# Kernel optimization log

Measured on AMD Instinct MI355X. Metric: run time of the kernel, lower is better.

The kernel has to match this reference:

```python
import jax, jax.numpy as jnp
import numpy as np

N = 100000   # nodes
E = 1600000  # edges
G = 512      # graphs
IN_F = 128
HID = 64
EPS = 1e-5


def setup_inputs() -> dict:
    key = jax.random.key(0)
    ks = jax.random.split(key, 16)
    x = jax.random.normal(ks[0], (N, IN_F), dtype=jnp.float32)
    edge_index = jax.random.randint(ks[1], (2, E), 0, N, dtype=jnp.int64)
    batch = jnp.sort(jax.random.randint(ks[2], (N,), 0, G, dtype=jnp.int64))
    s = 0.05
    return {
        'x': x, 'edge_index': edge_index, 'batch': batch,
        'W1': jax.random.normal(ks[3], (IN_F, HID), jnp.float32) * s,
        'b1': jax.random.normal(ks[4], (HID,), jnp.float32) * s,
        'g1': jax.random.uniform(ks[5], (HID,), jnp.float32),
        'be1': jax.random.normal(ks[6], (HID,), jnp.float32) * s,
        'rm1': jnp.zeros((HID,), jnp.float32),
        'rv1': jnp.ones((HID,), jnp.float32),
        'W2': jax.random.normal(ks[7], (HID, HID), jnp.float32) * s,
        'b2': jax.random.normal(ks[8], (HID,), jnp.float32) * s,
        'g2': jax.random.uniform(ks[9], (HID,), jnp.float32),
        'be2': jax.random.normal(ks[10], (HID,), jnp.float32) * s,
        'rm2': jnp.zeros((HID,), jnp.float32),
        'rv2': jnp.ones((HID,), jnp.float32),
        'Wh1': jax.random.normal(ks[11], (2 * HID, HID), jnp.float32) * s,
        'bh1': jax.random.normal(ks[12], (HID,), jnp.float32) * s,
        'Wh2': jax.random.normal(ks[13], (HID, HID // 2), jnp.float32) * s,
        'bh2': jnp.zeros((HID // 2,), jnp.float32),
        'Wh3': jax.random.normal(ks[14], (HID // 2, 1), jnp.float32) * s,
        'bh3': jnp.zeros((1,), jnp.float32),
    }


def _gcn(h, W, b, src, dst):
    # GCNConv with added self-loops and symmetric D^{-1/2} A D^{-1/2} normalization
    hw = h @ W                                   # [N, HID]
    deg = jnp.ones((N,), hw.dtype).at[dst].add(1.0)  # in-degree + self-loop
    dinv = jax.lax.rsqrt(deg)
    norm = dinv[src] * dinv[dst]                 # [E]
    agg = jax.ops.segment_sum(hw[src] * norm[:, None], dst, num_segments=N)
    return agg + hw * (dinv * dinv)[:, None] + b  # self-loop term + bias


def _bn(x, g, b, rm, rv):
    return (x - rm) * jax.lax.rsqrt(rv + EPS) * g + b


def reference(x, edge_index, batch, W1, b1, g1, be1, rm1, rv1,
              W2, b2, g2, be2, rm2, rv2, Wh1, bh1, Wh2, bh2, Wh3, bh3):
    src, dst = edge_index[0], edge_index[1]
    # layer 0 (no residual: dim change 128 -> 64)
    h = jax.nn.relu(_bn(_gcn(x, W1, b1, src, dst), g1, be1, rm1, rv1))
    # layer 1 with residual
    h = h + jax.nn.relu(_bn(_gcn(h, W2, b2, src, dst), g2, be2, rm2, rv2))
    # global mean + max pooling per graph
    ones = jnp.ones((N,), h.dtype)
    cnt = jnp.maximum(jax.ops.segment_sum(ones, batch, num_segments=G), 1.0)
    h_mean = jax.ops.segment_sum(h, batch, num_segments=G) / cnt[:, None]
    h_max = jax.ops.segment_max(h, batch, num_segments=G)
    hg = jnp.concatenate([h_mean, h_max], axis=-1)   # [G, 2*HID]
    # MLP head (dropout disabled in eval)
    z = jax.nn.relu(hg @ Wh1 + bh1)
    z = jax.nn.relu(z @ Wh2 + bh2)
    out = z @ Wh3 + bh3
    return jax.nn.sigmoid(out).squeeze(-1)           # [G]
```

## Files before the change

kernel.cpp:

```cpp
#include <hip/hip_runtime.h>
#include <math.h>

#define NN 100000
#define EE 1600000
#define GG 512
#define INF_ 128
#define HID 64
#define EPS 1e-5f

#define NBUK 391
#define P1_TILES 98
#define SETUP_B 25
#define POOL_WORDS (GG * 64 * 2 + GG)
#define ZERO_B ((POOL_WORDS + 255) / 256)

typedef unsigned int uint32;
typedef __attribute__((ext_vector_type(8))) short bf16x8;
typedef __attribute__((ext_vector_type(4))) float f32x4;

static __device__ inline uint32 f2bf(float f) {
    uint32 u = __float_as_uint(f);
    return (u + 0x7FFFu + ((u >> 16) & 1u)) >> 16;
}
static __device__ inline float bf_lo(uint32 u) { return __uint_as_float(u << 16); }
static __device__ inline float bf_hi(uint32 u) { return __uint_as_float(u & 0xFFFF0000u); }



__global__ __launch_bounds__(256) void k_hist1(const int* __restrict__ ei,
        int* __restrict__ hblk,
        const float* b1, const float* g1, const float* be1,
        const float* rm1, const float* rv1,
        const float* b2, const float* g2, const float* be2,
        const float* rm2, const float* rv2, float* sc,
        const float* W1, uint32* Wt1b, const float* W2, uint32* Wt2b,
        uint32* hwb, float* poolz) {
    int b = blockIdx.x, t = threadIdx.x;
    if (b < P1_TILES) {
        __shared__ int h[NBUK];
        for (int i = t; i < NBUK; i += 256) h[i] = 0;
        __syncthreads();
        const int4* dst4 = (const int4*)(ei + EE);
        int base4 = b * 4096;
        for (int j = 0; j < 16; ++j) {
            int i4 = base4 + j * 256 + t;
            if (i4 < EE / 4) {
                int4 d = dst4[i4];
                atomicAdd(&h[d.x >> 8], 1);
                atomicAdd(&h[d.y >> 8], 1);
                atomicAdd(&h[d.z >> 8], 1);
                atomicAdd(&h[d.w >> 8], 1);
            }
        }
        __syncthreads();
        for (int i = t; i < NBUK; i += 256) hblk[i * P1_TILES + b] = h[i];
    } else if (b < P1_TILES + SETUP_B) {
        int i = (b - P1_TILES) * 256 + t;
        if (i < 4096) {
            int n = i >> 6, kp = (i & 63) * 2;
            Wt1b[i] = f2bf(W1[(size_t)kp * 64 + n]) |
                      (f2bf(W1[(size_t)(kp + 1) * 64 + n]) << 16);
        } else if (i < 6144) {
            int j = i - 4096;
            int n = j >> 5, kp = (j & 31) * 2;
            Wt2b[j] = f2bf(W2[(size_t)kp * 64 + n]) |
                      (f2bf(W2[(size_t)(kp + 1) * 64 + n]) << 16);
        } else if (i < 6208) {
            int l = i - 6144;
            float s1 = g1[l] * rsqrtf(rv1[l] + EPS);
            sc[l]       = s1;
            sc[64 + l]  = (b1[l] - rm1[l]) * s1 + be1[l];
            float s2 = g2[l] * rsqrtf(rv2[l] + EPS);
            sc[128 + l] = s2;
            sc[192 + l] = (b2[l] - rm2[l]) * s2 + be2[l];
        } else if (i < 6240) {
            hwb[(size_t)NN * 32 + (i - 6208)] = 0u;
        }
    } else {
        int i = (b - P1_TILES - SETUP_B) * 256 + t;
        if (i < POOL_WORDS) poolz[i] = 0.f;
    }
}

__global__ void k_scan2(const int* __restrict__ hblk, int* __restrict__ bbase,
                        int* __restrict__ rbase, int* __restrict__ offs) {
    __shared__ int wsum[8];
    int t = threadIdx.x;
    int lane = t & 63, w = t >> 6;
    int c = 0;
    if (t < NBUK)
        for (int b = 0; b < P1_TILES; ++b) c += hblk[t * P1_TILES + b];
    int v = c;
    for (int d = 1; d < 64; d <<= 1) { int n = __shfl_up(v, d); if (lane >= d) v += n; }
    if (lane == 63) wsum[w] = v;
    __syncthreads();
    int pre = 0;
    for (int q = 0; q < w; ++q) pre += wsum[q];
    int excl = pre + v - c;
    if (t <= NBUK) bbase[t] = excl;
    if (t == 0) offs[NN] = EE;
    if (t < NBUK) {
        int run = excl;
        for (int b = 0; b < P1_TILES; ++b) {
            rbase[t * P1_TILES + b] = run;
            run += hblk[t * P1_TILES + b];
        }
    }
}

__global__ __launch_bounds__(256) void k_p1b(const int* __restrict__ ei,
                                             const int* __restrict__ rbase,
                                             uint32* __restrict__ pairs) {
    __shared__ int h[NBUK];
    int b = blockIdx.x, t = threadIdx.x;
    for (int i = t; i < NBUK; i += 256) h[i] = rbase[i * P1_TILES + b];
    __syncthreads();
    const int4* src4 = (const int4*)ei;
    const int4* dst4 = (const int4*)(ei + EE);
    int base4 = b * 4096;
    for (int j = 0; j < 16; ++j) {
        int i4 = base4 + j * 256 + t;
        if (i4 < EE / 4) {
            int4 d = dst4[i4];
            int4 s = src4[i4];
            int p0 = atomicAdd(&h[d.x >> 8], 1);
            pairs[p0] = ((uint32)s.x << 8) | (uint32)(d.x & 255);
            int p1 = atomicAdd(&h[d.y >> 8], 1);
            pairs[p1] = ((uint32)s.y << 8) | (uint32)(d.y & 255);
            int p2 = atomicAdd(&h[d.z >> 8], 1);
            pairs[p2] = ((uint32)s.z << 8) | (uint32)(d.z & 255);
            int p3 = atomicAdd(&h[d.w >> 8], 1);
            pairs[p3] = ((uint32)s.w << 8) | (uint32)(d.w & 255);
        }
    }
}

__global__ __launch_bounds__(256) void k_p2(const uint32* __restrict__ pairs,
                                            const int* __restrict__ bbase,
                                            int* __restrict__ offs, float* __restrict__ dinv,
                                            int* __restrict__ col) {
    int b = blockIdx.x, t = threadIdx.x;
    int nbase = b << 8;
    int ebase = bbase[b], eend = bbase[b + 1];
    int m = eend - ebase;
    __shared__ int cnt[256];
    __shared__ int wsum[4];
    cnt[t] = 0;
    __syncthreads();
    for (int i = t; i < m; i += 256)
        atomicAdd(&cnt[pairs[ebase + i] & 255u], 1);
    __syncthreads();
    int c = cnt[t];
    int lane = t & 63, w = t >> 6;
    int v = c;
    for (int d = 1; d < 64; d <<= 1) { int n = __shfl_up(v, d); if (lane >= d) v += n; }
    if (lane == 63) wsum[w] = v;
    __syncthreads();
    int pre = 0;
    for (int q = 0; q < w; ++q) pre += wsum[q];
    int excl = pre + v - c;
    int node = nbase + t;
    if (node < NN) {
        offs[node] = ebase + excl;
        dinv[node] = rsqrtf(1.f + (float)c);
    }
    __syncthreads();
    cnt[t] = excl;
    __syncthreads();
    for (int i = t; i < m; i += 256) {
        uint32 u = pairs[ebase + i];
        int loc = atomicAdd(&cnt[u & 255u], 1);
        col[ebase + loc] = (int)(u >> 8);
    }
}

template <int K>
__global__ __launch_bounds__(256) void k_gemm_mfma(const float* __restrict__ X,
                                                   const uint32* __restrict__ Wtb,
                                                   const float* __restrict__ dinv,
                                                   uint32* __restrict__ outb, int nrows) {
    constexpr int KP = K + 8;
    __shared__ alignas(16) unsigned short Al[64 * KP];
    __shared__ alignas(16) unsigned short Bl[64 * KP];
    int tid = threadIdx.x;
    for (int i = tid; i < 64 * (K / 2); i += 256) {
        int n = i / (K / 2), kp = i % (K / 2);
        *(uint32*)&Bl[n * KP + kp * 2] = Wtb[i];
    }
    int r0 = blockIdx.x * 64;
    const float* Xb = X + (size_t)r0 * K;
    int limit = (nrows - r0) * K;
    for (int f = tid * 4; f < 64 * K; f += 1024) {
        float4 v = {0.f, 0.f, 0.f, 0.f};
        if (f + 3 < limit) v = *(const float4*)&Xb[f];
        int row = f / K, kpos = f % K;
        ushort4 pk;
        pk.x = (unsigned short)f2bf(v.x);
        pk.y = (unsigned short)f2bf(v.y);
        pk.z = (unsigned short)f2bf(v.z);
        pk.w = (unsigned short)f2bf(v.w);
        *(ushort4*)&Al[row * KP + kpos] = pk;
    }
    __syncthreads();
    int lane = tid & 63, wv = tid >> 6;
    int m = lane & 15, quad = lane >> 4;
    f32x4 acc0 = {0.f, 0.f, 0.f, 0.f}, acc1 = acc0, acc2 = acc0, acc3 = acc0;
    int arow = wv * 16 + m;
#pragma unroll
    for (int k0 = 0; k0 < K; k0 += 32) {
        int koff = k0 + quad * 8;
        bf16x8 a = *(const bf16x8*)&Al[arow * KP + koff];
        bf16x8 b0 = *(const bf16x8*)&Bl[(0 * 16 + m) * KP + koff];
        bf16x8 b1 = *(const bf16x8*)&Bl[(1 * 16 + m) * KP + koff];
        bf16x8 b2 = *(const bf16x8*)&Bl[(2 * 16 + m) * KP + koff];
        bf16x8 b3 = *(const bf16x8*)&Bl[(3 * 16 + m) * KP + koff];
        acc0 = __builtin_amdgcn_mfma_f32_16x16x32_bf16(a, b0, acc0, 0, 0, 0);
        acc1 = __builtin_amdgcn_mfma_f32_16x16x32_bf16(a, b1, acc1, 0, 0, 0);
        acc2 = __builtin_amdgcn_mfma_f32_16x16x32_bf16(a, b2, acc2, 0, 0, 0);
        acc3 = __builtin_amdgcn_mfma_f32_16x16x32_bf16(a, b3, acc3, 0, 0, 0);
    }
    float dsc[4];
#pragma unroll
    for (int reg = 0; reg < 4; ++reg) {
        int row = r0 + wv * 16 + quad * 4 + reg;
        dsc[reg] = (row < nrows) ? dinv[row] : 0.f;
    }
    const float* accs[4] = {(const float*)&acc0, (const float*)&acc1,
                            (const float*)&acc2, (const float*)&acc3};
#pragma unroll
    for (int nt = 0; nt < 4; ++nt) {
#pragma unroll
        for (int reg = 0; reg < 4; ++reg) {
            float val = accs[nt][reg] * dsc[reg];
            float nxt = __shfl_down(val, 1);
            int row = r0 + wv * 16 + quad * 4 + reg;
            if (((m & 1) == 0) && row < nrows)
                outb[(size_t)row * 32 + nt * 8 + (m >> 1)] =
                    f2bf(val) | (f2bf(nxt) << 16);
        }
    }
}

__global__ void k_gcn_gather(const uint32* __restrict__ hwb, const int* __restrict__ col,
                             const int* __restrict__ offs,
                             const float* __restrict__ dinv, const float* __restrict__ scale,
                             const float* __restrict__ shift, const float* __restrict__ resid,
                             float* __restrict__ out) {
    int node = blockIdx.x * 4 + (threadIdx.x >> 6);
    if (node >= NN) return;
    int lane = threadIdx.x & 63;
    int q = lane >> 4;
    int fl = lane & 15;
    const uint2* hw2 = (const uint2*)hwb;
    int e0 = offs[node], e1 = offs[node + 1];
    float di = dinv[node];
    float a0 = 0.f, a1 = 0.f, a2 = 0.f, a3 = 0.f;
    float c0 = 0.f, c1 = 0.f, c2 = 0.f, c3 = 0.f;
    for (int base = e0; base < e1; base += 64) {
        int m = e1 - base; if (m > 64) m = 64;
        int srcv = NN;
        if (lane < m) srcv = col[base + lane];
        for (int j = 0; j < m; j += 16) {
            int sa = __shfl(srcv, j + q);
            int sb = __shfl(srcv, j + 4 + q);
            int sc = __shfl(srcv, j + 8 + q);
            int sd = __shfl(srcv, j + 12 + q);
            uint2 ua = hw2[(size_t)sa * 16 + fl];
            uint2 ub = hw2[(size_t)sb * 16 + fl];
            uint2 uc = hw2[(size_t)sc * 16 + fl];
            uint2 ud = hw2[(size_t)sd * 16 + fl];
            a0 += bf_lo(ua.x); a1 += bf_hi(ua.x); a2 += bf_lo(ua.y); a3 += bf_hi(ua.y);
            c0 += bf_lo(ub.x); c1 += bf_hi(ub.x); c2 += bf_lo(ub.y); c3 += bf_hi(ub.y);
            a0 += bf_lo(uc.x); a1 += bf_hi(uc.x); a2 += bf_lo(uc.y); a3 += bf_hi(uc.y);
            c0 += bf_lo(ud.x); c1 += bf_hi(ud.x); c2 += bf_lo(ud.y); c3 += bf_hi(ud.y);
        }
    }
    a0 += c0; a1 += c1; a2 += c2; a3 += c3;
    a0 += __shfl_xor(a0, 16); a1 += __shfl_xor(a1, 16);
    a2 += __shfl_xor(a2, 16); a3 += __shfl_xor(a3, 16);
    a0 += __shfl_xor(a0, 32); a1 += __shfl_xor(a1, 32);
    a2 += __shfl_xor(a2, 32); a3 += __shfl_xor(a3, 32);
    if (q == 0) {
        uint2 us = hw2[(size_t)node * 16 + fl];
        a0 += bf_lo(us.x); a1 += bf_hi(us.x);
        a2 += bf_lo(us.y); a3 += bf_hi(us.y);
        float4 sc4 = *(const float4*)&scale[4 * fl];
        float4 sh4 = *(const float4*)&shift[4 * fl];
        float v0 = fmaxf(fmaf(a0 * di, sc4.x, sh4.x), 0.f);
        float v1 = fmaxf(fmaf(a1 * di, sc4.y, sh4.y), 0.f);
        float v2 = fmaxf(fmaf(a2 * di, sc4.z, sh4.z), 0.f);
        float v3 = fmaxf(fmaf(a3 * di, sc4.w, sh4.w), 0.f);
        size_t oidx = (size_t)node * 64 + 4 * fl;
        if (resid) {
            float4 rv = *(const float4*)&resid[oidx];
            v0 += rv.x; v1 += rv.y; v2 += rv.z; v3 += rv.w;
        }
        float4 o; o.x = v0; o.y = v1; o.z = v2; o.w = v3;
        *(float4*)&out[oidx] = o;
    }
}

__global__ __launch_bounds__(256) void k_pool(const float* __restrict__ h,
                       const int* __restrict__ batch,
                       float* __restrict__ msum, float* __restrict__ mmax,
                       float* __restrict__ gcnt) {
    int lane = threadIdx.x & 63;
    int wv = threadIdx.x >> 6;
    int i0 = blockIdx.x * 128 + wv * 32;
    if (i0 >= NN) return;
    int i1 = i0 + 32; if (i1 > NN) i1 = NN;
    int cur = batch[i0];
    float sum = 0.f, mx = 0.f; int c = 0;
    for (int i = i0; i < i1; ++i) {
        int g = batch[i];
        if (g != cur) {
            atomicAdd(&msum[cur * 64 + lane], sum);
            atomicMax((unsigned int*)&mmax[cur * 64 + lane], __float_as_uint(mx));
            if (lane == 0) atomicAdd(&gcnt[cur], (float)c);
            sum = 0.f; mx = 0.f; c = 0; cur = g;
        }
        float v = h[(long)i * 64 + lane];
        sum += v; mx = fmaxf(mx, v); ++c;
    }
    atomicAdd(&msum[cur * 64 + lane], sum);
    atomicMax((unsigned int*)&mmax[cur * 64 + lane], __float_as_uint(mx));
    if (lane == 0) atomicAdd(&gcnt[cur], (float)c);
}

__global__ void k_head(const float* __restrict__ msum, const float* __restrict__ mmax,
                       const float* __restrict__ gcnt,
                       const float* __restrict__ Wh1, const float* __restrict__ bh1,
                       const float* __restrict__ Wh2, const float* __restrict__ bh2,
                       const float* __restrict__ Wh3, const float* __restrict__ bh3,
                       float* __restrict__ out) {
    int g = blockIdx.x, t = threadIdx.x;
    __shared__ float hg[128];
    __shared__ float z1[64];
    __shared__ float z2[32];
    float c = fmaxf(gcnt[g], 1.f);
    hg[t]      = msum[g * 64 + t] / c;
    hg[64 + t] = mmax[g * 64 + t];
    __syncthreads();
    float acc = bh1[t];
#pragma unroll 8
    for (int k = 0; k < 128; ++k) acc = fmaf(hg[k], Wh1[k * 64 + t], acc);
    z1[t] = fmaxf(acc, 0.f);
    __syncthreads();
    if (t < 32) {
        float a2 = bh2[t];
#pragma unroll 8
        for (int k = 0; k < 64; ++k) a2 = fmaf(z1[k], Wh2[k * 32 + t], a2);
        z2[t] = fmaxf(a2, 0.f);
    }
    __syncthreads();
    if (t == 0) {
        float a3 = bh3[0];
        for (int k = 0; k < 32; ++k) a3 = fmaf(z2[k], Wh3[k], a3);
        out[g] = 1.f / (1.f + expf(-a3));
    }
}


static inline size_t alignup(size_t x) { return (x + 255) & ~(size_t)255; }

extern "C" void kernel_launch(void* const* d_in, const int* in_sizes, int n_in,
                              void* d_out, int out_size, void* d_ws, size_t ws_size,
                              hipStream_t stream) {
    const float* x   = (const float*)d_in[0];
    const int*   ei  = (const int*)d_in[1];
    const int*   bat = (const int*)d_in[2];
    const float* W1  = (const float*)d_in[3];
    const float* b1  = (const float*)d_in[4];
    const float* g1  = (const float*)d_in[5];
    const float* be1 = (const float*)d_in[6];
    const float* rm1 = (const float*)d_in[7];
    const float* rv1 = (const float*)d_in[8];
    const float* W2  = (const float*)d_in[9];
    const float* b2  = (const float*)d_in[10];
    const float* g2  = (const float*)d_in[11];
    const float* be2 = (const float*)d_in[12];
    const float* rm2 = (const float*)d_in[13];
    const float* rv2 = (const float*)d_in[14];
    const float* Wh1 = (const float*)d_in[15];
    const float* bh1 = (const float*)d_in[16];
    const float* Wh2 = (const float*)d_in[17];
    const float* bh2 = (const float*)d_in[18];
    const float* Wh3 = (const float*)d_in[19];
    const float* bh3 = (const float*)d_in[20];
    float* out = (float*)d_out;

    char* ws = (char*)d_ws;
    size_t o = 0;
    int*   hblk   = (int*)(ws + o);  o = alignup(o + (size_t)P1_TILES * NBUK * 4);
    int*   rbase  = (int*)(ws + o);  o = alignup(o + (size_t)P1_TILES * NBUK * 4);
    int*   bbase  = (int*)(ws + o);  o = alignup(o + (NBUK + 1) * 4);
    int*   offs   = (int*)(ws + o);  o = alignup(o + (NN + 1) * 4);
    uint32* pairs = (uint32*)(ws + o); o = alignup(o + (size_t)EE * 4);
    int*   col    = (int*)(ws + o);  o = alignup(o + (size_t)EE * 4);
    float* dinv   = (float*)(ws + o); o = alignup(o + (size_t)NN * 4);
    float* scb    = (float*)(ws + o); o = alignup(o + 4 * 64 * 4);
    uint32* Wt1b  = (uint32*)(ws + o); o = alignup(o + 64 * (INF_ / 2) * 4);
    uint32* Wt2b  = (uint32*)(ws + o); o = alignup(o + 64 * (HID / 2) * 4);
    float* msum   = (float*)(ws + o); o += (size_t)GG * 64 * 4;
    float* mmax   = (float*)(ws + o); o += (size_t)GG * 64 * 4;
    float* gcnt   = (float*)(ws + o); o += (size_t)GG * 4;
    o = alignup(o);
    uint32* hwb   = (uint32*)(ws + o); o = alignup(o + ((size_t)NN + 1) * 32 * 4);
    float* h      = (float*)(ws + o); o = alignup(o + (size_t)NN * 64 * 4);
    (void)ws_size; (void)n_in; (void)in_sizes; (void)out_size;

    k_hist1<<<P1_TILES + SETUP_B + ZERO_B, 256, 0, stream>>>(
        ei, hblk, b1, g1, be1, rm1, rv1, b2, g2, be2, rm2, rv2, scb,
        W1, Wt1b, W2, Wt2b, hwb, msum);
    k_scan2<<<1, 512, 0, stream>>>(hblk, bbase, rbase, offs);
    k_p1b<<<P1_TILES, 256, 0, stream>>>(ei, rbase, pairs);
    k_p2<<<NBUK, 256, 0, stream>>>(pairs, bbase, offs, dinv, col);

    k_gemm_mfma<INF_><<<(NN + 63) / 64, 256, 0, stream>>>(x, Wt1b, dinv, hwb, NN);
    k_gcn_gather<<<(NN + 3) / 4, 256, 0, stream>>>(hwb, col, offs, dinv,
                                                   scb, scb + 64, nullptr, h);
    k_gemm_mfma<HID><<<(NN + 63) / 64, 256, 0, stream>>>(h, Wt2b, dinv, hwb, NN);
    k_gcn_gather<<<(NN + 3) / 4, 256, 0, stream>>>(hwb, col, offs, dinv,
                                                   scb + 128, scb + 192, h, h);
    k_pool<<<(NN + 127) / 128, 256, 0, stream>>>(h, bat, msum, mmax, gcnt);
    k_head<<<GG, 64, 0, stream>>>(msum, mmax, gcnt, Wh1, bh1, Wh2, bh2, Wh3, bh3, out);
}
```

Measured before the change: 312.2 us.

## Store intermediate node features in bf16 and regather with 32-lane half-wave layout

The hidden activations h are now stored as packed bf16 pairs instead of fp32. The second GEMM reads them directly without conversion, and pooling reads half the bytes. The gather kernel is restructured so that each half-wave covers all 64 features with one 32-bit load per lane and 8 edges in flight per iteration, replacing the earlier quarter-wave uint2 layout. This cuts memory traffic for writing and reading h, at the cost of extra rounding in the residual path and in pooling.

```diff
diff --git a/kernel.cpp b/kernel.cpp
--- a/kernel.cpp
+++ b/kernel.cpp
@@ -174,8 +174,8 @@
     }
 }
 
-template <int K>
-__global__ __launch_bounds__(256) void k_gemm_mfma(const float* __restrict__ X,
+template <int K, int XBF16>
+__global__ __launch_bounds__(256) void k_gemm_mfma(const void* __restrict__ Xv,
                                                    const uint32* __restrict__ Wtb,
                                                    const float* __restrict__ dinv,
                                                    uint32* __restrict__ outb, int nrows) {
@@ -188,18 +188,28 @@
         *(uint32*)&Bl[n * KP + kp * 2] = Wtb[i];
     }
     int r0 = blockIdx.x * 64;
-    const float* Xb = X + (size_t)r0 * K;
-    int limit = (nrows - r0) * K;
-    for (int f = tid * 4; f < 64 * K; f += 1024) {
-        float4 v = {0.f, 0.f, 0.f, 0.f};
-        if (f + 3 < limit) v = *(const float4*)&Xb[f];
-        int row = f / K, kpos = f % K;
-        ushort4 pk;
-        pk.x = (unsigned short)f2bf(v.x);
-        pk.y = (unsigned short)f2bf(v.y);
-        pk.z = (unsigned short)f2bf(v.z);
-        pk.w = (unsigned short)f2bf(v.w);
-        *(ushort4*)&Al[row * KP + kpos] = pk;
+    if (XBF16 == 0) {
+        const float* Xb = (const float*)Xv + (size_t)r0 * K;
+        int limit = (nrows - r0) * K;
+        for (int f = tid * 4; f < 64 * K; f += 1024) {
+            float4 v = {0.f, 0.f, 0.f, 0.f};
+            if (f + 3 < limit) v = *(const float4*)&Xb[f];
+            int row = f / K, kpos = f % K;
+            ushort4 pk;
+            pk.x = (unsigned short)f2bf(v.x);
+            pk.y = (unsigned short)f2bf(v.y);
+            pk.z = (unsigned short)f2bf(v.z);
+            pk.w = (unsigned short)f2bf(v.w);
+            *(ushort4*)&Al[row * KP + kpos] = pk;
+        }
+    } else {
+        const uint32* Xb = (const uint32*)Xv;
+        for (int i = tid; i < 64 * (K / 2); i += 256) {
+            int row = i / (K / 2), c = i % (K / 2);
+            uint32 v = 0;
+            if (r0 + row < nrows) v = Xb[(size_t)(r0 + row) * (K / 2) + c];
+            *(uint32*)&Al[row * KP + 2 * c] = v;
+        }
     }
     __syncthreads();
     int lane = tid & 63, wv = tid >> 6;
@@ -244,87 +254,95 @@
 __global__ void k_gcn_gather(const uint32* __restrict__ hwb, const int* __restrict__ col,
                              const int* __restrict__ offs,
                              const float* __restrict__ dinv, const float* __restrict__ scale,
-                             const float* __restrict__ shift, const float* __restrict__ resid,
-                             float* __restrict__ out) {
+                             const float* __restrict__ shift, const uint32* __restrict__ resid,
+                             uint32* __restrict__ outb) {
     int node = blockIdx.x * 4 + (threadIdx.x >> 6);
     if (node >= NN) return;
     int lane = threadIdx.x & 63;
-    int q = lane >> 4;
-    int fl = lane & 15;
-    const uint2* hw2 = (const uint2*)hwb;
+    int half = lane >> 5;
+    int fl = lane & 31;
     int e0 = offs[node], e1 = offs[node + 1];
     float di = dinv[node];
-    float a0 = 0.f, a1 = 0.f, a2 = 0.f, a3 = 0.f;
-    float c0 = 0.f, c1 = 0.f, c2 = 0.f, c3 = 0.f;
+    float ax0 = 0.f, ay0 = 0.f, ax1 = 0.f, ay1 = 0.f;
     for (int base = e0; base < e1; base += 64) {
         int m = e1 - base; if (m > 64) m = 64;
         int srcv = NN;
         if (lane < m) srcv = col[base + lane];
         for (int j = 0; j < m; j += 16) {
-            int sa = __shfl(srcv, j + q);
-            int sb = __shfl(srcv, j + 4 + q);
-            int sc = __shfl(srcv, j + 8 + q);
-            int sd = __shfl(srcv, j + 12 + q);
-            uint2 ua = hw2[(size_t)sa * 16 + fl];
-            uint2 ub = hw2[(size_t)sb * 16 + fl];
-            uint2 uc = hw2[(size_t)sc * 16 + fl];
-            uint2 ud = hw2[(size_t)sd * 16 + fl];
-            a0 += bf_lo(ua.x); a1 += bf_hi(ua.x); a2 += bf_lo(ua.y); a3 += bf_hi(ua.y);
-            c0 += bf_lo(ub.x); c1 += bf_hi(ub.x); c2 += bf_lo(ub.y); c3 += bf_hi(ub.y);
-            a0 += bf_lo(uc.x); a1 += bf_hi(uc.x); a2 += bf_lo(uc.y); a3 += bf_hi(uc.y);
-            c0 += bf_lo(ud.x); c1 += bf_hi(ud.x); c2 += bf_lo(ud.y); c3 += bf_hi(ud.y);
-        }
-    }
-    a0 += c0; a1 += c1; a2 += c2; a3 += c3;
-    a0 += __shfl_xor(a0, 16); a1 += __shfl_xor(a1, 16);
-    a2 += __shfl_xor(a2, 16); a3 += __shfl_xor(a3, 16);
-    a0 += __shfl_xor(a0, 32); a1 += __shfl_xor(a1, 32);
-    a2 += __shfl_xor(a2, 32); a3 += __shfl_xor(a3, 32);
-    if (q == 0) {
-        uint2 us = hw2[(size_t)node * 16 + fl];
-        a0 += bf_lo(us.x); a1 += bf_hi(us.x);
-        a2 += bf_lo(us.y); a3 += bf_hi(us.y);
-        float4 sc4 = *(const float4*)&scale[4 * fl];
-        float4 sh4 = *(const float4*)&shift[4 * fl];
-        float v0 = fmaxf(fmaf(a0 * di, sc4.x, sh4.x), 0.f);
-        float v1 = fmaxf(fmaf(a1 * di, sc4.y, sh4.y), 0.f);
-        float v2 = fmaxf(fmaf(a2 * di, sc4.z, sh4.z), 0.f);
-        float v3 = fmaxf(fmaf(a3 * di, sc4.w, sh4.w), 0.f);
-        size_t oidx = (size_t)node * 64 + 4 * fl;
+            int s0 = __shfl(srcv, j + half);
+            int s1 = __shfl(srcv, j + 2 + half);
+            int s2 = __shfl(srcv, j + 4 + half);
+            int s3 = __shfl(srcv, j + 6 + half);
+            int s4 = __shfl(srcv, j + 8 + half);
+            int s5 = __shfl(srcv, j + 10 + half);
+            int s6 = __shfl(srcv, j + 12 + half);
+            int s7 = __shfl(srcv, j + 14 + half);
+            uint32 u0 = hwb[(size_t)s0 * 32 + fl];
+            uint32 u1 = hwb[(size_t)s1 * 32 + fl];
+            uint32 u2 = hwb[(size_t)s2 * 32 + fl];
+            uint32 u3 = hwb[(size_t)s3 * 32 + fl];
+            uint32 u4 = hwb[(size_t)s4 * 32 + fl];
+            uint32 u5 = hwb[(size_t)s5 * 32 + fl];
+            uint32 u6 = hwb[(size_t)s6 * 32 + fl];
+            uint32 u7 = hwb[(size_t)s7 * 32 + fl];
+            ax0 += bf_lo(u0); ay0 += bf_hi(u0);
+            ax1 += bf_lo(u1); ay1 += bf_hi(u1);
+            ax0 += bf_lo(u2); ay0 += bf_hi(u2);
+            ax1 += bf_lo(u3); ay1 += bf_hi(u3);
+            ax0 += bf_lo(u4); ay0 += bf_hi(u4);
+            ax1 += bf_lo(u5); ay1 += bf_hi(u5);
+            ax0 += bf_lo(u6); ay0 += bf_hi(u6);
+            ax1 += bf_lo(u7); ay1 += bf_hi(u7);
+        }
+    }
+    float ax = ax0 + ax1, ay = ay0 + ay1;
+    ax += __shfl(ax, fl + 32);
+    ay += __shfl(ay, fl + 32);
+    if (half == 0) {
+        uint32 uself = hwb[(size_t)node * 32 + fl];
+        ax += bf_lo(uself); ay += bf_hi(uself);
+        float vx = fmaf(ax * di, scale[2 * fl],     shift[2 * fl]);
+        float vy = fmaf(ay * di, scale[2 * fl + 1], shift[2 * fl + 1]);
+        vx = fmaxf(vx, 0.f);
+        vy = fmaxf(vy, 0.f);
         if (resid) {
-            float4 rv = *(const float4*)&resid[oidx];
-            v0 += rv.x; v1 += rv.y; v2 += rv.z; v3 += rv.w;
-        }
-        float4 o; o.x = v0; o.y = v1; o.z = v2; o.w = v3;
-        *(float4*)&out[oidx] = o;
-    }
-}
-
-__global__ __launch_bounds__(256) void k_pool(const float* __restrict__ h,
+            uint32 rv = resid[(size_t)node * 32 + fl];
+            vx += bf_lo(rv); vy += bf_hi(rv);
+        }
+        outb[(size_t)node * 32 + fl] = f2bf(vx) | (f2bf(vy) << 16);
+    }
+}
+
+__global__ __launch_bounds__(256) void k_pool(const uint32* __restrict__ hb,
                        const int* __restrict__ batch,
                        float* __restrict__ msum, float* __restrict__ mmax,
                        float* __restrict__ gcnt) {
-    int lane = threadIdx.x & 63;
-    int wv = threadIdx.x >> 6;
-    int i0 = blockIdx.x * 128 + wv * 32;
+    int l = threadIdx.x & 31;
+    int hf = threadIdx.x >> 5;
+    int i0 = blockIdx.x * 256 + hf * 32;
     if (i0 >= NN) return;
     int i1 = i0 + 32; if (i1 > NN) i1 = NN;
     int cur = batch[i0];
-    float sum = 0.f, mx = 0.f; int c = 0;
+    float s0 = 0.f, s1 = 0.f, m0 = 0.f, m1 = 0.f; int c = 0;
     for (int i = i0; i < i1; ++i) {
         int g = batch[i];
         if (g != cur) {
-            atomicAdd(&msum[cur * 64 + lane], sum);
-            atomicMax((unsigned int*)&mmax[cur * 64 + lane], __float_as_uint(mx));
-            if (lane == 0) atomicAdd(&gcnt[cur], (float)c);
-            sum = 0.f; mx = 0.f; c = 0; cur = g;
-        }
-        float v = h[(long)i * 64 + lane];
-        sum += v; mx = fmaxf(mx, v); ++c;
-    }
-    atomicAdd(&msum[cur * 64 + lane], sum);
-    atomicMax((unsigned int*)&mmax[cur * 64 + lane], __float_as_uint(mx));
-    if (lane == 0) atomicAdd(&gcnt[cur], (float)c);
+            atomicAdd(&msum[cur * 64 + 2 * l], s0);
+            atomicAdd(&msum[cur * 64 + 2 * l + 1], s1);
+            atomicMax((unsigned int*)&mmax[cur * 64 + 2 * l], __float_as_uint(m0));
+            atomicMax((unsigned int*)&mmax[cur * 64 + 2 * l + 1], __float_as_uint(m1));
+            if (l == 0) atomicAdd(&gcnt[cur], (float)c);
+            s0 = s1 = m0 = m1 = 0.f; c = 0; cur = g;
+        }
+        uint32 u = hb[(size_t)i * 32 + l];
+        float vx = bf_lo(u), vy = bf_hi(u);
+        s0 += vx; s1 += vy; m0 = fmaxf(m0, vx); m1 = fmaxf(m1, vy); ++c;
+    }
+    atomicAdd(&msum[cur * 64 + 2 * l], s0);
+    atomicAdd(&msum[cur * 64 + 2 * l + 1], s1);
+    atomicMax((unsigned int*)&mmax[cur * 64 + 2 * l], __float_as_uint(m0));
+    atomicMax((unsigned int*)&mmax[cur * 64 + 2 * l + 1], __float_as_uint(m1));
+    if (l == 0) atomicAdd(&gcnt[cur], (float)c);
 }
 
 __global__ void k_head(const float* __restrict__ msum, const float* __restrict__ mmax,
@@ -406,7 +424,7 @@
     float* gcnt   = (float*)(ws + o); o += (size_t)GG * 4;
     o = alignup(o);
     uint32* hwb   = (uint32*)(ws + o); o = alignup(o + ((size_t)NN + 1) * 32 * 4);
-    float* h      = (float*)(ws + o); o = alignup(o + (size_t)NN * 64 * 4);
+    uint32* hb    = (uint32*)(ws + o); o = alignup(o + (size_t)NN * 32 * 4);
     (void)ws_size; (void)n_in; (void)in_sizes; (void)out_size;
 
     k_hist1<<<P1_TILES + SETUP_B + ZERO_B, 256, 0, stream>>>(
@@ -416,12 +434,12 @@
     k_p1b<<<P1_TILES, 256, 0, stream>>>(ei, rbase, pairs);
     k_p2<<<NBUK, 256, 0, stream>>>(pairs, bbase, offs, dinv, col);
 
-    k_gemm_mfma<INF_><<<(NN + 63) / 64, 256, 0, stream>>>(x, Wt1b, dinv, hwb, NN);
+    k_gemm_mfma<INF_, 0><<<(NN + 63) / 64, 256, 0, stream>>>(x, Wt1b, dinv, hwb, NN);
     k_gcn_gather<<<(NN + 3) / 4, 256, 0, stream>>>(hwb, col, offs, dinv,
-                                                   scb, scb + 64, nullptr, h);
-    k_gemm_mfma<HID><<<(NN + 63) / 64, 256, 0, stream>>>(h, Wt2b, dinv, hwb, NN);
+                                                   scb, scb + 64, nullptr, hb);
+    k_gemm_mfma<HID, 1><<<(NN + 63) / 64, 256, 0, stream>>>(hb, Wt2b, dinv, hwb, NN);
     k_gcn_gather<<<(NN + 3) / 4, 256, 0, stream>>>(hwb, col, offs, dinv,
-                                                   scb + 128, scb + 192, h, h);
-    k_pool<<<(NN + 127) / 128, 256, 0, stream>>>(h, bat, msum, mmax, gcnt);
+                                                   scb + 128, scb + 192, hb, hb);
+    k_pool<<<(NN + 255) / 256, 256, 0, stream>>>(hb, bat, msum, mmax, gcnt);
     k_head<<<GG, 64, 0, stream>>>(msum, mmax, gcnt, Wh1, bh1, Wh2, bh2, Wh3, bh3, out);
 }
```

Result: no change. 317.0 us (+1.6%).
